# Optimization experiments

Hardware: AMD Instinct MI355X
Metric: run time of the kernel (lower is better)

Reference implementation:

```python
import jax, jax.numpy as jnp
import numpy as np

SEQ_LEN = 32768
HID = 1024


def setup_inputs() -> dict:
    key = jax.random.key(0)
    k1, k2, k3, k4 = jax.random.split(key, 4)
    hidden = jax.random.normal(k1, (1, 1, HID), dtype=jnp.float32)
    encoder_outputs = jax.random.normal(k2, (SEQ_LEN, HID), dtype=jnp.float32)
    # nn.Linear(hidden_size, hidden_size): weight [H, H], bias [H]
    W = jax.random.normal(k3, (HID, HID), dtype=jnp.float32) * (1.0 / np.sqrt(HID))
    b = jax.random.normal(k4, (HID,), dtype=jnp.float32) * 0.01
    return {"hidden": hidden, "encoder_outputs": encoder_outputs, "W": W, "b": b}


def reference(hidden, encoder_outputs, W, b):
    # method == 'general':
    #   energy_i = Linear(enc_i) = W @ enc_i + b     -> [S, H]
    #   e_i = sum(hidden[-1, 0] * energy_i)           -> [S]
    h = hidden[-1, 0]                                 # [H]
    proj = jnp.einsum('sh,dh->sd', encoder_outputs, W) + b  # [S, H]
    energies = proj @ h                               # [S]
    attn = jax.nn.softmax(energies, axis=0)           # [S]
    return attn[None, None, :]                        # [1, 1, S]
```

## Files before the change

### kernel.cpp

```cpp
#include <hip/hip_runtime.h>
#include <math.h>

#define HID 1024
#define NBLK 1024
#define RLX __ATOMIC_RELAXED
#define AGT __HIP_MEMORY_SCOPE_AGENT

__device__ unsigned g_ctl[1152];
#define SUB(g)   ((g) << 5)
#define MASTER   1024
#define FLAG     1056
#define DEPART   1088

__device__ __forceinline__ unsigned ld32(const unsigned* p) { return __hip_atomic_load(p, RLX, AGT); }
__device__ __forceinline__ void st32(unsigned* p, unsigned v) { __hip_atomic_store(p, v, RLX, AGT); }
__device__ __forceinline__ unsigned long long ld64(const unsigned long long* p) { return __hip_atomic_load(p, RLX, AGT); }
__device__ __forceinline__ void st64(unsigned long long* p, unsigned long long v) { __hip_atomic_store(p, v, RLX, AGT); }
__device__ __forceinline__ unsigned add32(unsigned* p, unsigned v) { return __hip_atomic_fetch_add(p, v, RLX, AGT); }
__device__ __forceinline__ void vfence() { asm volatile("s_waitcnt vmcnt(0)" ::: "memory"); }
__device__ __forceinline__ void spin(unsigned* f) {
    for (int i = 0; i < (1 << 24); ++i) {
        if (ld32(f)) return;
        __builtin_amdgcn_s_sleep(2);
    }
}
__device__ __forceinline__ void mzmerge(float& m, float& z, float m2, float z2) {
    const float M = fmaxf(m, m2);
    z = z * __expf(m - M) + z2 * __expf(m2 - M);
    m = M;
}

__global__ void __launch_bounds__(256) k_matvec(const float* __restrict__ W,
                                                const float* __restrict__ hvec,
                                                float* __restrict__ v) {
    const int col = blockIdx.x;
    const int t = threadIdx.x;
    float acc = 0.f;
#pragma unroll
    for (int i = 0; i < 4; ++i) {
        const int d = (i << 8) + t;
        acc = fmaf(hvec[d], W[d * HID + col], acc);
    }
#pragma unroll
    for (int off = 32; off; off >>= 1) acc += __shfl_xor(acc, off, 64);
    __shared__ float red[4];
    if ((t & 63) == 0) red[t >> 6] = acc;
    __syncthreads();
    if (t == 0) v[col] = (red[0] + red[1]) + (red[2] + red[3]);
}

__global__ void __launch_bounds__(256)
k_energy(const float* __restrict__ enc, const float* __restrict__ v,
         unsigned* __restrict__ eglob, unsigned long long* __restrict__ bstats,
         unsigned long long* __restrict__ fstat, float* __restrict__ out) {
    const int t = threadIdx.x, bid = blockIdx.x;
    const int wave = t >> 6, lane = t & 63;

    __shared__ float wm[4], wz[4];
    __shared__ float e_lds[32];
    __shared__ float sm[256], sz[256];
    __shared__ int s_role;
    __shared__ float2 s_mz;

    {
        const int row0 = (bid << 5) + (wave << 3);
        const float4 vr0 = *reinterpret_cast<const float4*>(v +       (lane << 2));
        const float4 vr1 = *reinterpret_cast<const float4*>(v + 256 + (lane << 2));
        const float4 vr2 = *reinterpret_cast<const float4*>(v + 512 + (lane << 2));
        const float4 vr3 = *reinterpret_cast<const float4*>(v + 768 + (lane << 2));

        float m = -__builtin_inff();
        float z = 0.f;

        const float4* p = reinterpret_cast<const float4*>(enc + (size_t)row0 * HID) + lane;
        float4 a = p[0], b = p[64], c = p[128], d = p[192];

#pragma unroll
        for (int r = 0; r < 8; ++r) {
            float4 na, nb, nc, nd;
            if (r < 7) {
                const float4* q = p + (size_t)(r + 1) * 256;
                na = q[0]; nb = q[64]; nc = q[128]; nd = q[192];
            }
            float acc = a.x * vr0.x + a.y * vr0.y + a.z * vr0.z + a.w * vr0.w
                      + b.x * vr1.x + b.y * vr1.y + b.z * vr1.z + b.w * vr1.w
                      + c.x * vr2.x + c.y * vr2.y + c.z * vr2.z + c.w * vr2.w
                      + d.x * vr3.x + d.y * vr3.y + d.z * vr3.z + d.w * vr3.w;
#pragma unroll
            for (int off = 32; off; off >>= 1) acc += __shfl_xor(acc, off, 64);
            if (!lane) e_lds[(wave << 3) + r] = acc;
            mzmerge(m, z, acc, 1.f);
            a = na; b = nb; c = nc; d = nd;
        }
        if (!lane) { wm[wave] = m; wz[wave] = z; }
    }
    __syncthreads();

    if (t < 32) st32(eglob + (bid << 5) + t, __float_as_uint(e_lds[t]));
    if (t == 0) {
        float M = wm[0], Z = wz[0];
        mzmerge(M, Z, wm[1], wz[1]);
        mzmerge(M, Z, wm[2], wz[2]);
        mzmerge(M, Z, wm[3], wz[3]);
        st64(bstats + bid, __builtin_bit_cast(unsigned long long, make_float2(M, Z)));
        vfence();
        int role = -1;
        if (add32(g_ctl + SUB(bid >> 5), 1u) == 31u)
            role = (int)add32(g_ctl + MASTER, 1u);
        s_role = role;
    }
    __syncthreads();
    const int role = s_role;
    if (role < 0) return;

    if (role == 31) {
        float m = -__builtin_inff(), z = 0.f;
#pragma unroll
        for (int i = 0; i < 4; ++i) {
            const unsigned long long bits = ld64(bstats + t + (i << 8));
            const float2 s = __builtin_bit_cast(float2, bits);
            mzmerge(m, z, s.x, s.y);
        }
        sm[t] = m; sz[t] = z;
        __syncthreads();
        for (int off = 128; off; off >>= 1) {
            if (t < off) {
                float m1 = sm[t], z1 = sz[t];
                mzmerge(m1, z1, sm[t + off], sz[t + off]);
                sm[t] = m1; sz[t] = z1;
            }
            __syncthreads();
        }
        if (t == 0) {
            st64(fstat, __builtin_bit_cast(unsigned long long, make_float2(sm[0], sz[0])));
            vfence();
            st32(g_ctl + FLAG, 1u);
        }
    } else {
        if (t == 0) spin(g_ctl + FLAG);
    }
    __syncthreads();
    if (t == 0) s_mz = __builtin_bit_cast(float2, ld64(fstat));
    __syncthreads();

    const float M = s_mz.x;
    const float rZ = 1.f / s_mz.y;
    const int base = role << 10;
#pragma unroll
    for (int i = 0; i < 4; ++i) {
        const int r = base + (i << 8) + t;
        const float e = __uint_as_float(ld32(eglob + r));
        out[r] = __expf(e - M) * rZ;
    }

    if (t == 0) {
        if (add32(g_ctl + DEPART, 1u) == 31u) {
#pragma unroll
            for (int g = 0; g < 32; ++g) st32(g_ctl + SUB(g), 0u);
            st32(g_ctl + MASTER, 0u);
            st32(g_ctl + FLAG, 0u);
            st32(g_ctl + DEPART, 0u);
        }
    }
}

extern "C" void kernel_launch(void* const* d_in, const int* in_sizes, int n_in,
                              void* d_out, int out_size, void* d_ws, size_t ws_size,
                              hipStream_t stream) {
    const float* hidden = (const float*)d_in[0];
    const float* enc    = (const float*)d_in[1];
    const float* W      = (const float*)d_in[2];

    float* ws = (float*)d_ws;
    float* v        = ws;
    unsigned* eglob = (unsigned*)(ws + HID);
    unsigned long long* bstats = (unsigned long long*)(ws + HID + 32768);
    unsigned long long* fstat  = bstats + 1024;

    k_matvec<<<HID, 256, 0, stream>>>(W, hidden, v);
    k_energy<<<NBLK, 256, 0, stream>>>(enc, v, eglob, bstats, fstat, (float*)d_out);
}
```

Baseline: 38.79 us.

## Fuse matvec into energy kernel with in-kernel flag barrier and smaller blocks

```diff
diff --git a/kernel.cpp b/kernel.cpp
--- a/kernel.cpp
+++ b/kernel.cpp
@@ -1,16 +1,22 @@
 #include <hip/hip_runtime.h>
 #include <math.h>
 
+#define SEQ_LEN 32768
 #define HID 1024
-#define NBLK 1024
+#define NBLK 2048
+#define SWZ 997
 #define RLX __ATOMIC_RELAXED
 #define AGT __HIP_MEMORY_SCOPE_AGENT
 
-__device__ unsigned g_ctl[1152];
-#define SUB(g)   ((g) << 5)
-#define MASTER   1024
-#define FLAG     1056
-#define DEPART   1088
+typedef float f32x4 __attribute__((ext_vector_type(4)));
+
+#define VDONE      0
+#define VFLAG(i)   (32 + ((i) << 5))
+#define SUB(g)     (2080 + ((g) << 5))
+#define MASTER     4128
+#define FLAGR(i)   (4160 + ((i) << 5))
+#define DEPART     4416
+__device__ unsigned g_ctl[4448];
 
 __device__ __forceinline__ unsigned ld32(const unsigned* p) { return __hip_atomic_load(p, RLX, AGT); }
 __device__ __forceinline__ void st32(unsigned* p, unsigned v) { __hip_atomic_store(p, v, RLX, AGT); }
@@ -21,7 +27,7 @@
 __device__ __forceinline__ void spin(unsigned* f) {
     for (int i = 0; i < (1 << 24); ++i) {
         if (ld32(f)) return;
-        __builtin_amdgcn_s_sleep(2);
+        __builtin_amdgcn_s_sleep(4);
     }
 }
 __device__ __forceinline__ void mzmerge(float& m, float& z, float m2, float z2) {
@@ -30,79 +36,102 @@
     m = M;
 }
 
-__global__ void __launch_bounds__(256) k_matvec(const float* __restrict__ W,
-                                                const float* __restrict__ hvec,
-                                                float* __restrict__ v) {
-    const int col = blockIdx.x;
-    const int t = threadIdx.x;
-    float acc = 0.f;
-#pragma unroll
-    for (int i = 0; i < 4; ++i) {
-        const int d = (i << 8) + t;
-        acc = fmaf(hvec[d], W[d * HID + col], acc);
-    }
-#pragma unroll
-    for (int off = 32; off; off >>= 1) acc += __shfl_xor(acc, off, 64);
-    __shared__ float red[4];
-    if ((t & 63) == 0) red[t >> 6] = acc;
-    __syncthreads();
-    if (t == 0) v[col] = (red[0] + red[1]) + (red[2] + red[3]);
-}
-
 __global__ void __launch_bounds__(256)
-k_energy(const float* __restrict__ enc, const float* __restrict__ v,
-         unsigned* __restrict__ eglob, unsigned long long* __restrict__ bstats,
-         unsigned long long* __restrict__ fstat, float* __restrict__ out) {
+k_all(const float* __restrict__ W, const float* __restrict__ hvec,
+      const float* __restrict__ enc, unsigned* __restrict__ vglob,
+      unsigned long long* __restrict__ bstats,
+      unsigned long long* __restrict__ fstat,
+      float* __restrict__ out) {
     const int t = threadIdx.x, bid = blockIdx.x;
     const int wave = t >> 6, lane = t & 63;
-
+    unsigned* eglob = (unsigned*)fstat + 2;
+
+    __shared__ float v_lds[HID];
     __shared__ float wm[4], wz[4];
-    __shared__ float e_lds[32];
     __shared__ float sm[256], sz[256];
     __shared__ int s_role;
     __shared__ float2 s_mz;
 
+    if (bid < 32) {
+        const int ct = t & 31, dt = t >> 5;
+        const int col = (bid << 5) + ct;
+        float acc = 0.f;
+        const int d0 = dt << 7;
+#pragma unroll 8
+        for (int i = 0; i < 128; ++i) {
+            const int d = d0 + i;
+            acc = fmaf(hvec[d], W[(size_t)d * HID + col], acc);
+        }
+        __shared__ float red[8][33];
+        red[dt][ct] = acc;
+        __syncthreads();
+        if (t < 32) {
+            float s = 0.f;
+#pragma unroll
+            for (int i = 0; i < 8; ++i) s += red[i][t];
+            st32(vglob + (bid << 5) + t, __float_as_uint(s));
+        }
+        __syncthreads();
+        if (t == 0) {
+            vfence();
+            if (add32(g_ctl + VDONE, 1u) == 31u) {
+#pragma unroll
+                for (int i = 0; i < 64; ++i) st32(g_ctl + VFLAG(i), 1u);
+            }
+        }
+    }
+
+    if (t == 0) spin(g_ctl + VFLAG(bid & 63));
+    __syncthreads();
+
+#pragma unroll
+    for (int i = 0; i < 4; ++i) {
+        const int idx = (i << 8) + t;
+        v_lds[idx] = __uint_as_float(ld32(vglob + idx));
+    }
+    __syncthreads();
+
+    const int chunk = (bid * SWZ) & (NBLK - 1);
     {
-        const int row0 = (bid << 5) + (wave << 3);
-        const float4 vr0 = *reinterpret_cast<const float4*>(v +       (lane << 2));
-        const float4 vr1 = *reinterpret_cast<const float4*>(v + 256 + (lane << 2));
-        const float4 vr2 = *reinterpret_cast<const float4*>(v + 512 + (lane << 2));
-        const float4 vr3 = *reinterpret_cast<const float4*>(v + 768 + (lane << 2));
+        const int row0 = (chunk << 4) + (wave << 2);
+        const f32x4 vr0 = *reinterpret_cast<const f32x4*>(v_lds +       (lane << 2));
+        const f32x4 vr1 = *reinterpret_cast<const f32x4*>(v_lds + 256 + (lane << 2));
+        const f32x4 vr2 = *reinterpret_cast<const f32x4*>(v_lds + 512 + (lane << 2));
+        const f32x4 vr3 = *reinterpret_cast<const f32x4*>(v_lds + 768 + (lane << 2));
 
         float m = -__builtin_inff();
         float z = 0.f;
 
-        const float4* p = reinterpret_cast<const float4*>(enc + (size_t)row0 * HID) + lane;
-        float4 a = p[0], b = p[64], c = p[128], d = p[192];
-
-#pragma unroll
-        for (int r = 0; r < 8; ++r) {
-            float4 na, nb, nc, nd;
-            if (r < 7) {
-                const float4* q = p + (size_t)(r + 1) * 256;
+        const f32x4* p = reinterpret_cast<const f32x4*>(enc + (size_t)row0 * HID) + lane;
+        f32x4 a = p[0], b = p[64], c = p[128], d = p[192];
+
+#pragma unroll
+        for (int r = 0; r < 4; ++r) {
+            f32x4 na, nb, nc, nd;
+            if (r < 3) {
+                const f32x4* q = p + (size_t)(r + 1) * 256;
                 na = q[0]; nb = q[64]; nc = q[128]; nd = q[192];
             }
-            float acc = a.x * vr0.x + a.y * vr0.y + a.z * vr0.z + a.w * vr0.w
-                      + b.x * vr1.x + b.y * vr1.y + b.z * vr1.z + b.w * vr1.w
-                      + c.x * vr2.x + c.y * vr2.y + c.z * vr2.z + c.w * vr2.w
-                      + d.x * vr3.x + d.y * vr3.y + d.z * vr3.z + d.w * vr3.w;
+            const f32x4 s4 = a * vr0 + b * vr1 + c * vr2 + d * vr3;
+            float acc = (s4.x + s4.y) + (s4.z + s4.w);
 #pragma unroll
             for (int off = 32; off; off >>= 1) acc += __shfl_xor(acc, off, 64);
-            if (!lane) e_lds[(wave << 3) + r] = acc;
-            mzmerge(m, z, acc, 1.f);
+            if (lane == 0) st32(eglob + row0 + r, __float_as_uint(acc));
+            const float nm = fmaxf(m, acc);
+            z = z * __expf(m - nm) + __expf(acc - nm);
+            m = nm;
             a = na; b = nb; c = nc; d = nd;
         }
-        if (!lane) { wm[wave] = m; wz[wave] = z; }
-    }
-    __syncthreads();
-
-    if (t < 32) st32(eglob + (bid << 5) + t, __float_as_uint(e_lds[t]));
+        if (lane == 0) { wm[wave] = m; wz[wave] = z; }
+    }
+    __syncthreads();
+
     if (t == 0) {
         float M = wm[0], Z = wz[0];
         mzmerge(M, Z, wm[1], wz[1]);
         mzmerge(M, Z, wm[2], wz[2]);
         mzmerge(M, Z, wm[3], wz[3]);
-        st64(bstats + bid, __builtin_bit_cast(unsigned long long, make_float2(M, Z)));
+        st64(bstats + chunk, __builtin_bit_cast(unsigned long long, make_float2(M, Z)));
         vfence();
         int role = -1;
         if (add32(g_ctl + SUB(bid >> 5), 1u) == 31u)
@@ -113,12 +142,11 @@
     const int role = s_role;
     if (role < 0) return;
 
-    if (role == 31) {
+    if (role == 63) {
         float m = -__builtin_inff(), z = 0.f;
 #pragma unroll
-        for (int i = 0; i < 4; ++i) {
-            const unsigned long long bits = ld64(bstats + t + (i << 8));
-            const float2 s = __builtin_bit_cast(float2, bits);
+        for (int i = 0; i < 8; ++i) {
+            const float2 s = __builtin_bit_cast(float2, ld64(bstats + t + (i << 8)));
             mzmerge(m, z, s.x, s.y);
         }
         sm[t] = m; sz[t] = z;
@@ -134,10 +162,11 @@
         if (t == 0) {
             st64(fstat, __builtin_bit_cast(unsigned long long, make_float2(sm[0], sz[0])));
             vfence();
-            st32(g_ctl + FLAG, 1u);
+#pragma unroll
+            for (int i = 0; i < 8; ++i) st32(g_ctl + FLAGR(i), 1u);
         }
     } else {
-        if (t == 0) spin(g_ctl + FLAG);
+        if (t == 0) spin(g_ctl + FLAGR(role & 7));
     }
     __syncthreads();
     if (t == 0) s_mz = __builtin_bit_cast(float2, ld64(fstat));
@@ -145,20 +174,23 @@
 
     const float M = s_mz.x;
     const float rZ = 1.f / s_mz.y;
-    const int base = role << 10;
-#pragma unroll
-    for (int i = 0; i < 4; ++i) {
-        const int r = base + (i << 8) + t;
-        const float e = __uint_as_float(ld32(eglob + r));
-        out[r] = __expf(e - M) * rZ;
-    }
+    const int base = role << 9;
+    const unsigned long long ebits =
+        ld64(reinterpret_cast<const unsigned long long*>(eglob) + (base >> 1) + t);
+    const float2 e = __builtin_bit_cast(float2, ebits);
+    float2 o;
+    o.x = __expf(e.x - M) * rZ;
+    o.y = __expf(e.y - M) * rZ;
+    *reinterpret_cast<float2*>(out + base + (t << 1)) = o;
 
     if (t == 0) {
-        if (add32(g_ctl + DEPART, 1u) == 31u) {
-#pragma unroll
-            for (int g = 0; g < 32; ++g) st32(g_ctl + SUB(g), 0u);
+        if (add32(g_ctl + DEPART, 1u) == 63u) {
+            st32(g_ctl + VDONE, 0u);
+#pragma unroll
+            for (int i = 0; i < 64; ++i) { st32(g_ctl + VFLAG(i), 0u); st32(g_ctl + SUB(i), 0u); }
             st32(g_ctl + MASTER, 0u);
-            st32(g_ctl + FLAG, 0u);
+#pragma unroll
+            for (int i = 0; i < 8; ++i) st32(g_ctl + FLAGR(i), 0u);
             st32(g_ctl + DEPART, 0u);
         }
     }
@@ -172,11 +204,10 @@
     const float* W      = (const float*)d_in[2];
 
     float* ws = (float*)d_ws;
-    float* v        = ws;
-    unsigned* eglob = (unsigned*)(ws + HID);
-    unsigned long long* bstats = (unsigned long long*)(ws + HID + 32768);
-    unsigned long long* fstat  = bstats + 1024;
-
-    k_matvec<<<HID, 256, 0, stream>>>(W, hidden, v);
-    k_energy<<<NBLK, 256, 0, stream>>>(enc, v, eglob, bstats, fstat, (float*)d_out);
-}
+    unsigned* vglob = (unsigned*)ws;
+    unsigned long long* bstats = (unsigned long long*)(ws + HID);
+    unsigned long long* fstat = bstats + 2048;
+
+    k_all<<<NBLK, 256, 0, stream>>>(W, hidden, enc, vglob, bstats, fstat,
+                                    (float*)d_out);
+}
```

Measured after the change: 40.84 us. +5.3%, slower.
